# Kernel tuning notes

Hardware: AMD Instinct MI355X
Metric: run time of the kernel (lower is better)

Reference implementation:

```python
import jax, jax.numpy as jnp
import numpy as np

N_NODES = 50000
N_EDGES = 800000
HIDDEN = 128
N_LAYERS = 3
EPS = 1e-5


def setup_inputs() -> dict:
    key = jax.random.key(0)
    ks = jax.random.split(key, 6)
    x = jax.random.normal(ks[0], (N_NODES, HIDDEN), dtype=jnp.float32)
    edge_index = jax.random.randint(ks[1], (2, N_EDGES), 0, N_NODES, dtype=jnp.int64)
    scale = 1.0 / np.sqrt(HIDDEN)
    Wl = jax.random.normal(ks[2], (N_LAYERS, HIDDEN, HIDDEN), dtype=jnp.float32) * scale
    bl = jnp.zeros((N_LAYERS, HIDDEN), dtype=jnp.float32)
    Wr = jax.random.normal(ks[3], (N_LAYERS, HIDDEN, HIDDEN), dtype=jnp.float32) * scale
    gamma = jnp.ones((N_LAYERS, HIDDEN), dtype=jnp.float32)
    beta = jnp.zeros((N_LAYERS, HIDDEN), dtype=jnp.float32)
    return {"x": x, "edge_index": edge_index, "Wl": Wl, "bl": bl,
            "Wr": Wr, "gamma": gamma, "beta": beta}


def reference(x, edge_index, Wl, bl, Wr, gamma, beta):
    # SAGEConv (mean aggr): out_i = Wl @ mean_{j in N(i)} x_j + bl + Wr @ x_i
    # followed by BatchNorm (batch stats), ReLU, residual (layers > 0).
    src, dst = edge_index[0], edge_index[1]
    N = x.shape[0]
    deg = jax.ops.segment_sum(jnp.ones((src.shape[0],), dtype=x.dtype), dst,
                              num_segments=N)
    inv_deg = (1.0 / jnp.maximum(deg, 1.0))[:, None]  # [N,1]; empty nbhd -> 0 agg
    for i in range(N_LAYERS):
        msg = x[src]                                            # [E,H] gather
        agg = jax.ops.segment_sum(msg, dst, num_segments=N) * inv_deg  # [N,H]
        h = agg @ Wl[i].T + bl[i] + x @ Wr[i].T                 # [N,H]
        mean = jnp.mean(h, axis=0)
        var = jnp.var(h, axis=0)                                # biased, as torch BN
        h = gamma[i] * (h - mean) * jax.lax.rsqrt(var + EPS) + beta[i]
        h = jax.nn.relu(h)
        x = h + x if i > 0 else h
    return x
```

## Files before the change

### kernel.cpp

```cpp
#include <hip/hip_runtime.h>

#define HH 128
#define EPS 1e-5f
#define NBMAX 256
#define SCAP 40
#define FCAP 12288

typedef __bf16 bf16x8 __attribute__((ext_vector_type(8)));
typedef float f32x4 __attribute__((ext_vector_type(4)));
typedef float f32x2 __attribute__((ext_vector_type(2)));

__device__ __forceinline__ unsigned f2bf(float f) {
    unsigned u = __builtin_bit_cast(unsigned, f);
    return (u + 0x7FFFu + ((u >> 16) & 1u)) >> 16;
}
__device__ __forceinline__ float bflo(unsigned w) { return __builtin_bit_cast(float, w << 16); }
__device__ __forceinline__ float bfhi(unsigned w) { return __builtin_bit_cast(float, w & 0xFFFF0000u); }

__device__ __forceinline__ unsigned pack_fp8x4(float f0, float f1, float f2, float f3) {
    unsigned r = 0;
    r = __builtin_amdgcn_cvt_pk_fp8_f32(f0, f1, r, false);
    r = __builtin_amdgcn_cvt_pk_fp8_f32(f2, f3, r, true);
    return r;
}

__device__ __forceinline__ void gload_lds16(const void* g, void* l) {
    __builtin_amdgcn_global_load_lds(
        (const __attribute__((address_space(1))) unsigned int*)g,
        (__attribute__((address_space(3))) unsigned int*)l,
        16, 0, 0);
}

__global__ void zero_small_kernel(int* __restrict__ bcnt, float* __restrict__ stats3) {
    const int t = threadIdx.x;
    bcnt[t] = 0;
    stats3[t] = 0.f; stats3[256 + t] = 0.f; stats3[512 + t] = 0.f;
}

__global__ __launch_bounds__(256) void bucket_hist_kernel(const int* __restrict__ dst,
                                                          int* __restrict__ bcnt, int E) {
    __shared__ int h[NBMAX];
    const int t = threadIdx.x;
    h[t] = 0;
    __syncthreads();
    for (int e = blockIdx.x * 256 + t; e < E; e += gridDim.x * 256)
        atomicAdd(&h[dst[e] >> 8], 1);
    __syncthreads();
    if (h[t]) atomicAdd(&bcnt[t], h[t]);
}

__global__ __launch_bounds__(256) void bucket_scan_kernel(const int* __restrict__ bcnt,
                                                          int* __restrict__ boff,
                                                          int* __restrict__ gpos, int NB, int E) {
    __shared__ int s[NBMAX];
    const int t = threadIdx.x;
    s[t] = (t < NB) ? bcnt[t] : 0;
    __syncthreads();
    for (int off = 1; off < 256; off <<= 1) {
        int u = (t >= off) ? s[t - off] : 0;
        __syncthreads();
        s[t] += u;
        __syncthreads();
    }
    int excl = (t == 0) ? 0 : s[t - 1];
    if (t < NB) { boff[t] = excl; gpos[t] = excl; }
    if (t == 0) boff[NB] = E;
}

__global__ __launch_bounds__(256) void bucket_scatter_kernel(
    const int* __restrict__ src, const int* __restrict__ dst,
    int* __restrict__ gpos, unsigned* __restrict__ packed, int E, int GRID)
{
    __shared__ unsigned q[NBMAX][SCAP];
    __shared__ int qc[NBMAX];
    const int t = threadIdx.x;
    const int b = blockIdx.x;
    qc[t] = 0;
    __syncthreads();
    const int ebeg = (int)((long)b * E / GRID);
    const int eend = (int)((long)(b + 1) * E / GRID);
    for (int base = ebeg; base < eend; base += 256) {
        int e = base + t;
        if (e < eend) {
            int d = dst[e];
            unsigned pk = ((unsigned)d << 16) | (unsigned)src[e];
            int bk = d >> 8;
            int slot = atomicAdd(&qc[bk], 1);
            if (slot < SCAP) q[bk][slot] = pk;
            else { int p = atomicAdd(&gpos[bk], 1); packed[p] = pk; }
        }
        __syncthreads();
        int c = qc[t]; if (c > SCAP) c = SCAP;
        if (c >= 32) {
            int p = atomicAdd(&gpos[t], 32);
            for (int i = 0; i < 32; ++i) packed[p + i] = q[t][i];
            for (int i = 32; i < c; ++i) q[t][i - 32] = q[t][i];
            qc[t] = c - 32;
        } else {
            qc[t] = c;
        }
        __syncthreads();
    }
    int c = qc[t]; if (c > SCAP) c = SCAP;
    if (c > 0) {
        int p = atomicAdd(&gpos[t], c);
        for (int i = 0; i < c; ++i) packed[p + i] = q[t][i];
    }
}

__global__ __launch_bounds__(256) void bucket_finalize_kernel(
    const unsigned* __restrict__ packed, const int* __restrict__ boff,
    int* __restrict__ row_ptr, float* __restrict__ invdeg,
    ushort* __restrict__ edge_csr, int N, int E)
{
    __shared__ int hist[256];
    __shared__ int posq[256];
    __shared__ ushort outq[FCAP];
    const int b = blockIdx.x, t = threadIdx.x;
    const int beg = boff[b], end = boff[b + 1], n = end - beg;
    hist[t] = 0;
    __syncthreads();
    for (int i = beg + t; i < end; i += 256)
        atomicAdd(&hist[(packed[i] >> 16) & 255], 1);
    __syncthreads();
    const int c = hist[t];
    for (int off = 1; off < 256; off <<= 1) {
        int u = (t >= off) ? hist[t - off] : 0;
        __syncthreads();
        hist[t] += u;
        __syncthreads();
    }
    const int excl = hist[t] - c;
    const int node = (b << 8) + t;
    if (node < N) {
        row_ptr[node] = beg + excl;
        invdeg[node] = 1.0f / fmaxf((float)c, 1.0f);
    }
    if (b == 0 && t == 0) row_ptr[N] = E;
    posq[t] = excl;
    __syncthreads();
    if (n <= FCAP) {
        for (int i = beg + t; i < end; i += 256) {
            unsigned pk = packed[i];
            int p = atomicAdd(&posq[(pk >> 16) & 255], 1);
            outq[p] = (ushort)(pk & 0xFFFFu);
        }
        __syncthreads();
        for (int i = t; i < n; i += 256) edge_csr[beg + i] = outq[i];
    } else {
        for (int i = beg + t; i < end; i += 256) {
            unsigned pk = packed[i];
            int p = atomicAdd(&posq[(pk >> 16) & 255], 1);
            edge_csr[beg + p] = (ushort)(pk & 0xFFFFu);
        }
    }
}

__global__ void convert_all_kernel(const float* __restrict__ x,
                                   const float* __restrict__ Wl, const float* __restrict__ Wr,
                                   ushort* __restrict__ xb, unsigned* __restrict__ xq,
                                   ushort* __restrict__ Wb,
                                   int n4, int m4, int wtotal) {
    int gid = blockIdx.x * 256 + threadIdx.x;
    if (gid < wtotal) {
        int l = gid / (HH * 256);
        int rem = gid - l * (HH * 256);
        int col = rem >> 8;
        int k = rem & 255;
        float v = (k < HH) ? Wl[(size_t)l * HH * HH + col * HH + k]
                           : Wr[(size_t)l * HH * HH + col * HH + (k - HH)];
        Wb[gid] = (ushort)f2bf(v);
        return;
    }
    int idx = gid - wtotal;
    if (idx >= m4) return;
    uint2 o = make_uint2(0u, 0u);
    unsigned q = 0u;
    if (idx < n4) {
        float4 v = ((const float4*)x)[idx];
        o.x = f2bf(v.x) | (f2bf(v.y) << 16);
        o.y = f2bf(v.z) | (f2bf(v.w) << 16);
        q = pack_fp8x4(v.x, v.y, v.z, v.w);
    }
    ((uint2*)xb)[idx] = o;
    xq[idx] = q;
}

__global__ __launch_bounds__(256) void gather_kernel(
    const unsigned* __restrict__ xq, const int* __restrict__ row_ptr,
    const ushort* __restrict__ edge_csr, const float* __restrict__ invdeg,
    ushort* __restrict__ aggb, int N)
{
    const int node = blockIdx.x * 16 + (threadIdx.x >> 4);
    const int l16 = threadIdx.x & 15;
    float a0=0,a1=0,a2=0,a3=0,a4=0,a5=0,a6=0,a7=0;
    float id = 0.f;
    if (node < N) {
        const int beg = row_ptr[node], end = row_ptr[node + 1];
        id = invdeg[node];
        int e = beg;
        for (; e + 3 < end; e += 4) {
            int s0 = edge_csr[e], s1 = edge_csr[e + 1];
            int s2 = edge_csr[e + 2], s3 = edge_csr[e + 3];
            uint2 v0 = *(const uint2*)(xq + (size_t)s0 * 32 + l16 * 2);
            uint2 v1 = *(const uint2*)(xq + (size_t)s1 * 32 + l16 * 2);
            uint2 v2 = *(const uint2*)(xq + (size_t)s2 * 32 + l16 * 2);
            uint2 v3 = *(const uint2*)(xq + (size_t)s3 * 32 + l16 * 2);
            f32x2 p;
            p = __builtin_amdgcn_cvt_pk_f32_fp8(v0.x, false); a0 += p.x; a1 += p.y;
            p = __builtin_amdgcn_cvt_pk_f32_fp8(v0.x, true);  a2 += p.x; a3 += p.y;
            p = __builtin_amdgcn_cvt_pk_f32_fp8(v0.y, false); a4 += p.x; a5 += p.y;
            p = __builtin_amdgcn_cvt_pk_f32_fp8(v0.y, true);  a6 += p.x; a7 += p.y;
            p = __builtin_amdgcn_cvt_pk_f32_fp8(v1.x, false); a0 += p.x; a1 += p.y;
            p = __builtin_amdgcn_cvt_pk_f32_fp8(v1.x, true);  a2 += p.x; a3 += p.y;
            p = __builtin_amdgcn_cvt_pk_f32_fp8(v1.y, false); a4 += p.x; a5 += p.y;
            p = __builtin_amdgcn_cvt_pk_f32_fp8(v1.y, true);  a6 += p.x; a7 += p.y;
            p = __builtin_amdgcn_cvt_pk_f32_fp8(v2.x, false); a0 += p.x; a1 += p.y;
            p = __builtin_amdgcn_cvt_pk_f32_fp8(v2.x, true);  a2 += p.x; a3 += p.y;
            p = __builtin_amdgcn_cvt_pk_f32_fp8(v2.y, false); a4 += p.x; a5 += p.y;
            p = __builtin_amdgcn_cvt_pk_f32_fp8(v2.y, true);  a6 += p.x; a7 += p.y;
            p = __builtin_amdgcn_cvt_pk_f32_fp8(v3.x, false); a0 += p.x; a1 += p.y;
            p = __builtin_amdgcn_cvt_pk_f32_fp8(v3.x, true);  a2 += p.x; a3 += p.y;
            p = __builtin_amdgcn_cvt_pk_f32_fp8(v3.y, false); a4 += p.x; a5 += p.y;
            p = __builtin_amdgcn_cvt_pk_f32_fp8(v3.y, true);  a6 += p.x; a7 += p.y;
        }
        for (; e < end; ++e) {
            int s0 = edge_csr[e];
            uint2 v0 = *(const uint2*)(xq + (size_t)s0 * 32 + l16 * 2);
            f32x2 p;
            p = __builtin_amdgcn_cvt_pk_f32_fp8(v0.x, false); a0 += p.x; a1 += p.y;
            p = __builtin_amdgcn_cvt_pk_f32_fp8(v0.x, true);  a2 += p.x; a3 += p.y;
            p = __builtin_amdgcn_cvt_pk_f32_fp8(v0.y, false); a4 += p.x; a5 += p.y;
            p = __builtin_amdgcn_cvt_pk_f32_fp8(v0.y, true);  a6 += p.x; a7 += p.y;
        }
    }
    uint4 o;
    o.x = f2bf(a0 * id) | (f2bf(a1 * id) << 16);
    o.y = f2bf(a2 * id) | (f2bf(a3 * id) << 16);
    o.z = f2bf(a4 * id) | (f2bf(a5 * id) << 16);
    o.w = f2bf(a6 * id) | (f2bf(a7 * id) << 16);
    *(uint4*)(aggb + (size_t)node * HH + l16 * 8) = o;
}

__global__ __launch_bounds__(512) void mfma_gemm_kernel(
    const ushort* __restrict__ aggb, const ushort* __restrict__ xb,
    const ushort* __restrict__ Wb, const float* __restrict__ bl,
    ushort* __restrict__ hb, float* __restrict__ stats, int N)
{
    __shared__ ushort As[64 * 256];
    __shared__ float s_sum[128];
    __shared__ float s_sum2[128];

    const int tid = threadIdx.x;
    const int lane = tid & 63;
    const int wave = tid >> 6;
    const int m0 = blockIdx.x * 64;
    const int l15 = lane & 15;
    const int lg = lane >> 4;
    const int col = wave * 16 + l15;

#pragma unroll
    for (int i = 0; i < 4; ++i) {
        const int cb = (i * 8 + wave) * 64;
        const int L = cb + lane;
        const int r = L >> 5;
        const int c = L & 31;
        const int cs = (c & 0x18) | ((c & 7) ^ (r & 7));
        const ushort* gsrc = (cs < 16)
            ? (aggb + (size_t)(m0 + r) * HH + cs * 8)
            : (xb   + (size_t)(m0 + r) * HH + (cs - 16) * 8);
        gload_lds16(gsrc, &As[(size_t)cb * 8]);
    }

    bf16x8 bfr[8];
#pragma unroll
    for (int s = 0; s < 8; ++s)
        bfr[s] = *(const bf16x8*)(Wb + (size_t)col * 256 + s * 32 + lg * 8);

    if (tid < 128) { s_sum[tid] = 0.f; s_sum2[tid] = 0.f; }

    f32x4 acc[4];
#pragma unroll
    for (int rt = 0; rt < 4; ++rt)
        acc[rt] = (f32x4){0.f, 0.f, 0.f, 0.f};

    __syncthreads();

#pragma unroll
    for (int s = 0; s < 8; ++s) {
#pragma unroll
        for (int rt = 0; rt < 4; ++rt) {
            const int r = rt * 16 + l15;
            const int g = s * 4 + lg;
            const int c = (g & 0x18) | ((g & 7) ^ (r & 7));
            bf16x8 a = *(const bf16x8*)&As[r * 256 + c * 8];
            acc[rt] = __builtin_amdgcn_mfma_f32_16x16x32_bf16(a, bfr[s], acc[rt], 0, 0, 0);
        }
    }

    __syncthreads();
    ushort* Cs = As;
    {
        const float bias = bl[col];
        float s1 = 0.f, s2 = 0.f;
#pragma unroll
        for (int rt = 0; rt < 4; ++rt) {
#pragma unroll
            for (int r = 0; r < 4; ++r) {
                const int row = rt * 16 + lg * 4 + r;
                float v = acc[rt][r] + bias;
                if (m0 + row < N) { s1 += v; s2 += v * v; }
                Cs[row * 136 + col] = (ushort)f2bf(v);
            }
        }
        atomicAdd(&s_sum[col], s1);
        atomicAdd(&s_sum2[col], s2);
    }
    __syncthreads();
#pragma unroll
    for (int i = 0; i < 2; ++i) {
        const int ch = tid + i * 512;
        const int row = ch >> 4;
        const int q = ch & 15;
        if (m0 + row < N) {
            uint4 v = *(const uint4*)&Cs[row * 136 + q * 8];
            *(uint4*)(hb + (size_t)(m0 + row) * HH + q * 8) = v;
        }
    }
    if (tid < 128) {
        atomicAdd(&stats[tid], s_sum[tid]);
        atomicAdd(&stats[128 + tid], s_sum2[tid]);
    }
}

__global__ __launch_bounds__(256) void bn_relu_res_kernel(
    const ushort* __restrict__ hb, const float* __restrict__ stats,
    const float* __restrict__ gamma, const float* __restrict__ beta, float invN,
    ushort* __restrict__ xb, unsigned* __restrict__ xq, float* __restrict__ outf,
    int n8, int residual, int final_layer)
{
    __shared__ float s_ab[256];
    const int t = threadIdx.x;
    if (t < 128) {
        float mean = stats[t] * invN;
        float var = stats[128 + t] * invN - mean * mean;
        float istd = rsqrtf(var + EPS);
        float a = gamma[t] * istd;
        s_ab[t] = a;
        s_ab[128 + t] = beta[t] - mean * a;
    }
    __syncthreads();
    int idx = blockIdx.x * 256 + t;
    if (idx >= n8) return;
    int f8 = idx & 15;
    uint4 hw = ((const uint4*)hb)[idx];
    float4 a0 = *(const float4*)&s_ab[f8 * 8];
    float4 a1 = *(const float4*)&s_ab[f8 * 8 + 4];
    float4 b0 = *(const float4*)&s_ab[128 + f8 * 8];
    float4 b1 = *(const float4*)&s_ab[128 + f8 * 8 + 4];
    float o0 = fmaxf(fmaf(bflo(hw.x), a0.x, b0.x), 0.f);
    float o1 = fmaxf(fmaf(bfhi(hw.x), a0.y, b0.y), 0.f);
    float o2 = fmaxf(fmaf(bflo(hw.y), a0.z, b0.z), 0.f);
    float o3 = fmaxf(fmaf(bfhi(hw.y), a0.w, b0.w), 0.f);
    float o4 = fmaxf(fmaf(bflo(hw.z), a1.x, b1.x), 0.f);
    float o5 = fmaxf(fmaf(bfhi(hw.z), a1.y, b1.y), 0.f);
    float o6 = fmaxf(fmaf(bflo(hw.w), a1.z, b1.z), 0.f);
    float o7 = fmaxf(fmaf(bfhi(hw.w), a1.w, b1.w), 0.f);
    if (residual) {
        uint4 xw = ((const uint4*)xb)[idx];
        o0 += bflo(xw.x); o1 += bfhi(xw.x);
        o2 += bflo(xw.y); o3 += bfhi(xw.y);
        o4 += bflo(xw.z); o5 += bfhi(xw.z);
        o6 += bflo(xw.w); o7 += bfhi(xw.w);
    }
    if (final_layer) {
        float4 f0 = make_float4(o0, o1, o2, o3);
        float4 f1 = make_float4(o4, o5, o6, o7);
        ((float4*)outf)[idx * 2] = f0;
        ((float4*)outf)[idx * 2 + 1] = f1;
    } else {
        uint4 ob;
        ob.x = f2bf(o0) | (f2bf(o1) << 16);
        ob.y = f2bf(o2) | (f2bf(o3) << 16);
        ob.z = f2bf(o4) | (f2bf(o5) << 16);
        ob.w = f2bf(o6) | (f2bf(o7) << 16);
        ((uint4*)xb)[idx] = ob;
        uint2 qb;
        qb.x = pack_fp8x4(o0, o1, o2, o3);
        qb.y = pack_fp8x4(o4, o5, o6, o7);
        ((uint2*)xq)[idx] = qb;
    }
}

extern "C" void kernel_launch(void* const* d_in, const int* in_sizes, int n_in,
                              void* d_out, int out_size, void* d_ws, size_t ws_size,
                              hipStream_t stream) {
    const float* x     = (const float*)d_in[0];
    const int*   ei    = (const int*)d_in[1];
    const float* Wl    = (const float*)d_in[2];
    const float* bl    = (const float*)d_in[3];
    const float* Wr    = (const float*)d_in[4];
    const float* gamma = (const float*)d_in[5];
    const float* beta  = (const float*)d_in[6];
    float* out = (float*)d_out;

    const int N = in_sizes[0] / HH;
    const int E = in_sizes[1] / 2;
    const int MP = ((N + 63) / 64) * 64;
    const int NB = (N + 255) >> 8;
    const int* src = ei;
    const int* dst = ei + E;

    char* p = (char*)d_ws;
    ushort* aggb    = (ushort*)p; p += (size_t)MP * HH * 2;
    ushort* xb      = (ushort*)p; p += (size_t)MP * HH * 2;
    unsigned* xq    = (unsigned*)p; p += (size_t)MP * 32 * 4;
    ushort* Wb      = (ushort*)p; p += (size_t)3 * HH * 256 * 2;
    float* invdeg   = (float*)p;  p += (size_t)N * 4;
    float* stats3   = (float*)p;  p += 768 * 4;
    int* row_ptr    = (int*)p;    p += (size_t)(N + 4) * 4;
    int* bcnt       = (int*)p;    p += NBMAX * 4;
    int* boff       = (int*)p;    p += (NBMAX + 1) * 4;
    int* gpos       = (int*)p;    p += NBMAX * 4;
    unsigned* packed = (unsigned*)p; p += (size_t)E * 4;
    ushort* edge_csr = (ushort*)p;  p += (size_t)((E + 7) & ~7) * 2;

    zero_small_kernel<<<1, 256, 0, stream>>>(bcnt, stats3);
    bucket_hist_kernel<<<512, 256, 0, stream>>>(dst, bcnt, E);
    bucket_scan_kernel<<<1, 256, 0, stream>>>(bcnt, boff, gpos, NB, E);
    bucket_scatter_kernel<<<256, 256, 0, stream>>>(src, dst, gpos, packed, E, 256);
    bucket_finalize_kernel<<<NB, 256, 0, stream>>>(packed, boff, row_ptr, invdeg, edge_csr, N, E);

    const int wtotal = 3 * HH * 256;
    const int n4 = N * (HH / 4);
    const int m4 = MP * (HH / 4);
    convert_all_kernel<<<(wtotal + m4 + 255) / 256, 256, 0, stream>>>(
        x, Wl, Wr, xb, xq, Wb, n4, m4, wtotal);

    const int gather_blocks = MP / 16;
    const int gemm_blocks = MP / 64;
    const int n8 = N * (HH / 8);
    const int elem_blocks = (n8 + 255) / 256;

    for (int layer = 0; layer < 3; ++layer) {
        float* stats = stats3 + layer * 256;

        gather_kernel<<<gather_blocks, 256, 0, stream>>>(
            xq, row_ptr, edge_csr, invdeg, aggb, N);

        mfma_gemm_kernel<<<gemm_blocks, 512, 0, stream>>>(
            aggb, xb, Wb + (size_t)layer * HH * 256,
            bl + (size_t)layer * HH,
            aggb , stats, N);

        bn_relu_res_kernel<<<elem_blocks, 256, 0, stream>>>(
            aggb , stats,
            gamma + (size_t)layer * HH, beta + (size_t)layer * HH, 1.0f / (float)N,
            xb, xq, out, n8, layer > 0 ? 1 : 0, layer == 2 ? 1 : 0);
    }
}
```

Measured before the change: 238.4 us.

## Fuse GEMM and BatchNorm/ReLU/residual via grid-wide barrier in one kernel

Merges the MFMA GEMM and the BN/ReLU/residual elementwise kernel into one persistent-style kernel. Each block now covers 256 rows and keeps its accumulators in registers, and a global atomic barrier waits until every block has contributed its column statistics. Blocks then apply the normalization in place and write xb/xq/out directly, which avoids the bf16 h round trip and one launch per layer. With 196 blocks of 512 threads and 128KB of LDS each, the barrier relies on all blocks being co-resident; if they are not, it deadlocks. The 16 accumulator tiles per thread also raise register pressure.

```diff
diff --git a/kernel.cpp b/kernel.cpp
--- a/kernel.cpp
+++ b/kernel.cpp
@@ -31,10 +31,12 @@
         16, 0, 0);
 }
 
-__global__ void zero_small_kernel(int* __restrict__ bcnt, float* __restrict__ stats3) {
+__global__ void zero_small_kernel(int* __restrict__ bcnt, float* __restrict__ stats3,
+                                  unsigned* __restrict__ bar3) {
     const int t = threadIdx.x;
     bcnt[t] = 0;
     stats3[t] = 0.f; stats3[256 + t] = 0.f; stats3[512 + t] = 0.f;
+    if (t < 3) bar3[t] = 0u;
 }
 
 __global__ __launch_bounds__(256) void bucket_hist_kernel(const int* __restrict__ dst,
@@ -242,25 +244,28 @@
     *(uint4*)(aggb + (size_t)node * HH + l16 * 8) = o;
 }
 
-__global__ __launch_bounds__(512) void mfma_gemm_kernel(
-    const ushort* __restrict__ aggb, const ushort* __restrict__ xb,
+__global__ __launch_bounds__(512) void fused_layer_kernel(
+    const ushort* __restrict__ aggb, ushort* __restrict__ xb,
     const ushort* __restrict__ Wb, const float* __restrict__ bl,
-    ushort* __restrict__ hb, float* __restrict__ stats, int N)
+    const float* __restrict__ gamma, const float* __restrict__ beta,
+    float* __restrict__ stats, unsigned* __restrict__ bar,
+    unsigned* __restrict__ xq, float* __restrict__ outf,
+    float invN, int nblocks, int N, int residual, int final_layer)
 {
-    __shared__ ushort As[64 * 256];
+    extern __shared__ ushort As[];
     __shared__ float s_sum[128];
     __shared__ float s_sum2[128];
 
     const int tid = threadIdx.x;
     const int lane = tid & 63;
     const int wave = tid >> 6;
-    const int m0 = blockIdx.x * 64;
+    const int m0 = blockIdx.x * 256;
     const int l15 = lane & 15;
     const int lg = lane >> 4;
     const int col = wave * 16 + l15;
 
 #pragma unroll
-    for (int i = 0; i < 4; ++i) {
+    for (int i = 0; i < 16; ++i) {
         const int cb = (i * 8 + wave) * 64;
         const int L = cb + lane;
         const int r = L >> 5;
@@ -279,17 +284,16 @@
 
     if (tid < 128) { s_sum[tid] = 0.f; s_sum2[tid] = 0.f; }
 
-    f32x4 acc[4];
-#pragma unroll
-    for (int rt = 0; rt < 4; ++rt)
-        acc[rt] = (f32x4){0.f, 0.f, 0.f, 0.f};
+    f32x4 acc[16];
+#pragma unroll
+    for (int rt = 0; rt < 16; ++rt) acc[rt] = (f32x4){0.f, 0.f, 0.f, 0.f};
 
     __syncthreads();
 
 #pragma unroll
     for (int s = 0; s < 8; ++s) {
 #pragma unroll
-        for (int rt = 0; rt < 4; ++rt) {
+        for (int rt = 0; rt < 16; ++rt) {
             const int r = rt * 16 + l15;
             const int g = s * 4 + lg;
             const int c = (g & 0x18) | ((g & 7) ^ (r & 7));
@@ -298,97 +302,90 @@
         }
     }
 
-    __syncthreads();
+    const float bias = bl[col];
+    float s1 = 0.f, s2 = 0.f;
+#pragma unroll
+    for (int rt = 0; rt < 16; ++rt) {
+#pragma unroll
+        for (int r = 0; r < 4; ++r) {
+            const int row = rt * 16 + lg * 4 + r;
+            if (m0 + row < N) {
+                float v = acc[rt][r] + bias;
+                s1 += v; s2 += v * v;
+            }
+        }
+    }
+    atomicAdd(&s_sum[col], s1);
+    atomicAdd(&s_sum2[col], s2);
+    __syncthreads();
+    if (tid < 128) {
+        atomicAdd(&stats[tid], s_sum[tid]);
+        atomicAdd(&stats[128 + tid], s_sum2[tid]);
+    }
+    if (tid == 0) {
+        __threadfence();
+        __hip_atomic_fetch_add(bar, 1u, __ATOMIC_ACQ_REL, __HIP_MEMORY_SCOPE_AGENT);
+        while (__hip_atomic_load(bar, __ATOMIC_ACQUIRE, __HIP_MEMORY_SCOPE_AGENT) < (unsigned)nblocks)
+            __builtin_amdgcn_s_sleep(8);
+    }
+    __syncthreads();
+
+    const float sA = __hip_atomic_load(&stats[col], __ATOMIC_RELAXED, __HIP_MEMORY_SCOPE_AGENT);
+    const float sB = __hip_atomic_load(&stats[128 + col], __ATOMIC_RELAXED, __HIP_MEMORY_SCOPE_AGENT);
+    const float mean = sA * invN;
+    const float var = sB * invN - mean * mean;
+    const float aa = gamma[col] * rsqrtf(var + EPS);
+    const float bb = beta[col] - mean * aa;
+
     ushort* Cs = As;
-    {
-        const float bias = bl[col];
-        float s1 = 0.f, s2 = 0.f;
-#pragma unroll
-        for (int rt = 0; rt < 4; ++rt) {
-#pragma unroll
-            for (int r = 0; r < 4; ++r) {
-                const int row = rt * 16 + lg * 4 + r;
-                float v = acc[rt][r] + bias;
-                if (m0 + row < N) { s1 += v; s2 += v * v; }
-                Cs[row * 136 + col] = (ushort)f2bf(v);
-            }
-        }
-        atomicAdd(&s_sum[col], s1);
-        atomicAdd(&s_sum2[col], s2);
-    }
-    __syncthreads();
-#pragma unroll
-    for (int i = 0; i < 2; ++i) {
+#pragma unroll
+    for (int rt = 0; rt < 16; ++rt) {
+#pragma unroll
+        for (int r = 0; r < 4; ++r) {
+            const int row = rt * 16 + lg * 4 + r;
+            float v = acc[rt][r] + bias;
+            float o = fmaxf(fmaf(v, aa, bb), 0.f);
+            Cs[row * 136 + col] = (ushort)f2bf(o);
+        }
+    }
+    __syncthreads();
+
+#pragma unroll
+    for (int i = 0; i < 8; ++i) {
         const int ch = tid + i * 512;
         const int row = ch >> 4;
         const int q = ch & 15;
-        if (m0 + row < N) {
+        const int grow = m0 + row;
+        if (grow < N) {
             uint4 v = *(const uint4*)&Cs[row * 136 + q * 8];
-            *(uint4*)(hb + (size_t)(m0 + row) * HH + q * 8) = v;
-        }
-    }
-    if (tid < 128) {
-        atomicAdd(&stats[tid], s_sum[tid]);
-        atomicAdd(&stats[128 + tid], s_sum2[tid]);
-    }
-}
-
-__global__ __launch_bounds__(256) void bn_relu_res_kernel(
-    const ushort* __restrict__ hb, const float* __restrict__ stats,
-    const float* __restrict__ gamma, const float* __restrict__ beta, float invN,
-    ushort* __restrict__ xb, unsigned* __restrict__ xq, float* __restrict__ outf,
-    int n8, int residual, int final_layer)
-{
-    __shared__ float s_ab[256];
-    const int t = threadIdx.x;
-    if (t < 128) {
-        float mean = stats[t] * invN;
-        float var = stats[128 + t] * invN - mean * mean;
-        float istd = rsqrtf(var + EPS);
-        float a = gamma[t] * istd;
-        s_ab[t] = a;
-        s_ab[128 + t] = beta[t] - mean * a;
-    }
-    __syncthreads();
-    int idx = blockIdx.x * 256 + t;
-    if (idx >= n8) return;
-    int f8 = idx & 15;
-    uint4 hw = ((const uint4*)hb)[idx];
-    float4 a0 = *(const float4*)&s_ab[f8 * 8];
-    float4 a1 = *(const float4*)&s_ab[f8 * 8 + 4];
-    float4 b0 = *(const float4*)&s_ab[128 + f8 * 8];
-    float4 b1 = *(const float4*)&s_ab[128 + f8 * 8 + 4];
-    float o0 = fmaxf(fmaf(bflo(hw.x), a0.x, b0.x), 0.f);
-    float o1 = fmaxf(fmaf(bfhi(hw.x), a0.y, b0.y), 0.f);
-    float o2 = fmaxf(fmaf(bflo(hw.y), a0.z, b0.z), 0.f);
-    float o3 = fmaxf(fmaf(bfhi(hw.y), a0.w, b0.w), 0.f);
-    float o4 = fmaxf(fmaf(bflo(hw.z), a1.x, b1.x), 0.f);
-    float o5 = fmaxf(fmaf(bfhi(hw.z), a1.y, b1.y), 0.f);
-    float o6 = fmaxf(fmaf(bflo(hw.w), a1.z, b1.z), 0.f);
-    float o7 = fmaxf(fmaf(bfhi(hw.w), a1.w, b1.w), 0.f);
-    if (residual) {
-        uint4 xw = ((const uint4*)xb)[idx];
-        o0 += bflo(xw.x); o1 += bfhi(xw.x);
-        o2 += bflo(xw.y); o3 += bfhi(xw.y);
-        o4 += bflo(xw.z); o5 += bfhi(xw.z);
-        o6 += bflo(xw.w); o7 += bfhi(xw.w);
-    }
-    if (final_layer) {
-        float4 f0 = make_float4(o0, o1, o2, o3);
-        float4 f1 = make_float4(o4, o5, o6, o7);
-        ((float4*)outf)[idx * 2] = f0;
-        ((float4*)outf)[idx * 2 + 1] = f1;
-    } else {
-        uint4 ob;
-        ob.x = f2bf(o0) | (f2bf(o1) << 16);
-        ob.y = f2bf(o2) | (f2bf(o3) << 16);
-        ob.z = f2bf(o4) | (f2bf(o5) << 16);
-        ob.w = f2bf(o6) | (f2bf(o7) << 16);
-        ((uint4*)xb)[idx] = ob;
-        uint2 qb;
-        qb.x = pack_fp8x4(o0, o1, o2, o3);
-        qb.y = pack_fp8x4(o4, o5, o6, o7);
-        ((uint2*)xq)[idx] = qb;
+            float o0 = bflo(v.x), o1 = bfhi(v.x);
+            float o2 = bflo(v.y), o3 = bfhi(v.y);
+            float o4 = bflo(v.z), o5 = bfhi(v.z);
+            float o6 = bflo(v.w), o7 = bfhi(v.w);
+            if (residual) {
+                uint4 xw = *(const uint4*)(xb + (size_t)grow * HH + q * 8);
+                o0 += bflo(xw.x); o1 += bfhi(xw.x);
+                o2 += bflo(xw.y); o3 += bfhi(xw.y);
+                o4 += bflo(xw.z); o5 += bfhi(xw.z);
+                o6 += bflo(xw.w); o7 += bfhi(xw.w);
+            }
+            if (final_layer) {
+                float* op = outf + (size_t)grow * HH + q * 8;
+                *(float4*)op = make_float4(o0, o1, o2, o3);
+                *(float4*)(op + 4) = make_float4(o4, o5, o6, o7);
+            } else {
+                uint4 ob;
+                ob.x = f2bf(o0) | (f2bf(o1) << 16);
+                ob.y = f2bf(o2) | (f2bf(o3) << 16);
+                ob.z = f2bf(o4) | (f2bf(o5) << 16);
+                ob.w = f2bf(o6) | (f2bf(o7) << 16);
+                *(uint4*)(xb + (size_t)grow * HH + q * 8) = ob;
+                uint2 qb;
+                qb.x = pack_fp8x4(o0, o1, o2, o3);
+                qb.y = pack_fp8x4(o4, o5, o6, o7);
+                *(uint2*)(xq + (size_t)grow * 32 + q * 2) = qb;
+            }
+        }
     }
 }
 
@@ -406,7 +403,7 @@
 
     const int N = in_sizes[0] / HH;
     const int E = in_sizes[1] / 2;
-    const int MP = ((N + 63) / 64) * 64;
+    const int MP = ((N + 255) / 256) * 256;
     const int NB = (N + 255) >> 8;
     const int* src = ei;
     const int* dst = ei + E;
@@ -418,6 +415,7 @@
     ushort* Wb      = (ushort*)p; p += (size_t)3 * HH * 256 * 2;
     float* invdeg   = (float*)p;  p += (size_t)N * 4;
     float* stats3   = (float*)p;  p += 768 * 4;
+    unsigned* bar3  = (unsigned*)p; p += 16 * 4;
     int* row_ptr    = (int*)p;    p += (size_t)(N + 4) * 4;
     int* bcnt       = (int*)p;    p += NBMAX * 4;
     int* boff       = (int*)p;    p += (NBMAX + 1) * 4;
@@ -425,7 +423,10 @@
     unsigned* packed = (unsigned*)p; p += (size_t)E * 4;
     ushort* edge_csr = (ushort*)p;  p += (size_t)((E + 7) & ~7) * 2;
 
-    zero_small_kernel<<<1, 256, 0, stream>>>(bcnt, stats3);
+    hipFuncSetAttribute((const void*)fused_layer_kernel,
+                        hipFuncAttributeMaxDynamicSharedMemorySize, 131072);
+
+    zero_small_kernel<<<1, 256, 0, stream>>>(bcnt, stats3, bar3);
     bucket_hist_kernel<<<512, 256, 0, stream>>>(dst, bcnt, E);
     bucket_scan_kernel<<<1, 256, 0, stream>>>(bcnt, boff, gpos, NB, E);
     bucket_scatter_kernel<<<256, 256, 0, stream>>>(src, dst, gpos, packed, E, 256);
@@ -438,24 +439,17 @@
         x, Wl, Wr, xb, xq, Wb, n4, m4, wtotal);
 
     const int gather_blocks = MP / 16;
-    const int gemm_blocks = MP / 64;
-    const int n8 = N * (HH / 8);
-    const int elem_blocks = (n8 + 255) / 256;
+    const int fused_blocks = MP / 256;
 
     for (int layer = 0; layer < 3; ++layer) {
-        float* stats = stats3 + layer * 256;
-
         gather_kernel<<<gather_blocks, 256, 0, stream>>>(
             xq, row_ptr, edge_csr, invdeg, aggb, N);
 
-        mfma_gemm_kernel<<<gemm_blocks, 512, 0, stream>>>(
-            aggb, xb, Wb + (size_t)layer * HH * 256,
-            bl + (size_t)layer * HH,
-            aggb , stats, N);
-
-        bn_relu_res_kernel<<<elem_blocks, 256, 0, stream>>>(
-            aggb , stats,
-            gamma + (size_t)layer * HH, beta + (size_t)layer * HH, 1.0f / (float)N,
-            xb, xq, out, n8, layer > 0 ? 1 : 0, layer == 2 ? 1 : 0);
-    }
-}
+        fused_layer_kernel<<<fused_blocks, 512, 131072, stream>>>(
+            aggb, xb, Wb + (size_t)layer * HH * 256, bl + (size_t)layer * HH,
+            gamma + (size_t)layer * HH, beta + (size_t)layer * HH,
+            stats3 + layer * 256, bar3 + layer,
+            xq, out, 1.0f / (float)N, fused_blocks, N,
+            layer > 0 ? 1 : 0, layer == 2 ? 1 : 0);
+    }
+}
```

Result: faster. 223.3 us (-6.3%).
